# Optimization experiments

Hardware: AMD Instinct MI355X
Metric: run time of the kernel (lower is better)

Reference implementation:

```python
import jax, jax.numpy as jnp
import numpy as np
import math

B, T, C = 4, 2048, 1024
D_ATTN, N_HEAD = 1024, 16
HEAD = D_ATTN // N_HEAD


def setup_inputs() -> dict:
    key = jax.random.key(0)
    k1, k2, k3 = jax.random.split(key, 3)
    x = jax.random.normal(k1, (B, T, C), dtype=jnp.float32)
    mask = jnp.tril(jnp.ones((T, T), dtype=jnp.int32))  # causal mask, 0 = blocked
    W_qkv = jax.random.normal(k2, (C, 3 * D_ATTN), dtype=jnp.float32) * (1.0 / math.sqrt(C))
    b_qkv = jnp.zeros((3 * D_ATTN,), dtype=jnp.float32)
    W_out = jax.random.normal(k3, (D_ATTN, C), dtype=jnp.float32) * (1.0 / math.sqrt(D_ATTN))
    b_out = jnp.zeros((C,), dtype=jnp.float32)
    return {"x": x, "mask": mask, "W_qkv": W_qkv, "b_qkv": b_qkv, "W_out": W_out, "b_out": b_out}


def reference(x, mask, W_qkv, b_qkv, W_out, b_out):
    Bx, Tx, Cx = x.shape
    qkv = x @ W_qkv + b_qkv                      # [B, T, 3*d_attn]
    q, k, v = jnp.split(qkv, 3, axis=-1)
    # [B, T, d_attn] -> [B, H, T, head]
    q = q.reshape(Bx, Tx, N_HEAD, HEAD).transpose(0, 2, 1, 3)
    k = k.reshape(Bx, Tx, N_HEAD, HEAD).transpose(0, 2, 1, 3)
    v = v.reshape(Bx, Tx, N_HEAD, HEAD).transpose(0, 2, 1, 3)
    scale = 1.0 / math.sqrt(HEAD)
    scores = jnp.einsum('bhqd,bhkd->bhqk', q, k) * scale  # [B, H, T, T]
    scores = jnp.where(mask == 0, -jnp.inf, scores)
    att = jax.nn.softmax(scores, axis=-1)
    out = jnp.einsum('bhqk,bhkd->bhqd', att, v)           # [B, H, T, head]
    out = out.transpose(0, 2, 1, 3).reshape(Bx, Tx, D_ATTN)
    return out @ W_out + b_out
```

## Files before the change

kernel.cpp:

```cpp
#include <hip/hip_runtime.h>

#define B_    4
#define T_    2048
#define C_    1024
#define DATTN 1024
#define NHEAD 16
#define M_    (B_*T_)
#define NQKV  (3*DATTN)

typedef __bf16 bf16;
typedef bf16  bf16x8 __attribute__((ext_vector_type(8)));
typedef bf16  bf16x4 __attribute__((ext_vector_type(4)));
typedef short s16x4  __attribute__((ext_vector_type(4)));
typedef float f32x4  __attribute__((ext_vector_type(4)));
typedef unsigned short u16x8 __attribute__((ext_vector_type(8)));

#define NEGBIG (-1e30f)
#define QSCALE (0.125f * 1.44269504088896f)

typedef const __attribute__((address_space(1))) unsigned int* gas_u32;
typedef __attribute__((address_space(3))) unsigned int* las_u32;

static __device__ __forceinline__ f32x4 mfma16(bf16x4 a, bf16x4 b, f32x4 c) {
#if __has_builtin(__builtin_amdgcn_mfma_f32_16x16x16bf16_1k)
    return __builtin_amdgcn_mfma_f32_16x16x16bf16_1k(
        __builtin_bit_cast(s16x4, a), __builtin_bit_cast(s16x4, b), c, 0, 0, 0);
#else
    asm("v_mfma_f32_16x16x16_bf16 %0, %1, %2, %0" : "+v"(c) : "v"(a), "v"(b));
    return c;
#endif
}

static __device__ __forceinline__ bf16x4 pk4(float a, float b, float c, float d) {
    union { unsigned int u[2]; bf16x4 v; } r;
    asm("v_cvt_pk_bf16_f32 %0, %1, %2" : "=v"(r.u[0]) : "v"(a), "v"(b));
    asm("v_cvt_pk_bf16_f32 %0, %1, %2" : "=v"(r.u[1]) : "v"(c), "v"(d));
    return r.v;
}

__global__ void detect_dtype(const unsigned short* __restrict__ x, int* flag) {
    __shared__ int cnt;
    if (threadIdx.x == 0) cnt = 0;
    __syncthreads();
    int local = 0;
    for (int j = 0; j < 8; ++j) {
        u16x8 v = *(const u16x8*)&x[(j * 256 + threadIdx.x) * 8];
        for (int k = 0; k < 8; ++k)
            if ((v[k] & 0x7F80) == 0x7F80) ++local;
    }
    atomicAdd(&cnt, local);
    __syncthreads();
    if (threadIdx.x == 0) *flag = (cnt > 0) ? 1 : 0;
}

__global__ void convert_x_any(const void* __restrict__ src, bf16* __restrict__ dst,
                              int n, const int* __restrict__ flag) {
    int i = (blockIdx.x * 256 + threadIdx.x) * 8;
    if (i >= n) return;
    if (*flag == 0) {
        *(bf16x8*)&dst[i] = *(const bf16x8*)((const bf16*)src + i);
    } else {
        const float* s = (const float*)src + i;
        f32x4 a = *(const f32x4*)s, b2 = *(const f32x4*)(s + 4);
        bf16x8 r;
        r[0] = (bf16)a[0]; r[1] = (bf16)a[1]; r[2] = (bf16)a[2]; r[3] = (bf16)a[3];
        r[4] = (bf16)b2[0]; r[5] = (bf16)b2[1]; r[6] = (bf16)b2[2]; r[7] = (bf16)b2[3];
        *(bf16x8*)&dst[i] = r;
    }
}

__global__ void prep_bias(const void* __restrict__ bq, const void* __restrict__ bo,
                          bf16* __restrict__ dq, bf16* __restrict__ do_,
                          const int* __restrict__ flag) {
    const int f = *flag;
    int i = blockIdx.x * 256 + threadIdx.x;
    if (i < NQKV) {
        float v = f ? ((const float*)bq)[i] : (float)((const bf16*)bq)[i];
        if (i < DATTN) v *= QSCALE;
        dq[i] = (bf16)v;
    } else if (i - NQKV < C_) {
        do_[i - NQKV] = f ? (bf16)((const float*)bo)[i - NQKV] : ((const bf16*)bo)[i - NQKV];
    }
}

__global__ void transpose_w_any(const void* __restrict__ src, bf16* __restrict__ dst,
                                int R, int C, const int* __restrict__ flag,
                                float scale, int scale_cols) {
    __shared__ bf16 tile[32][33];
    const int f = *flag;
    const int c0 = blockIdx.x * 32, r0 = blockIdx.y * 32;
    const int tx = threadIdx.x & 31, ty = threadIdx.x >> 5;
    const float s = (c0 + tx < scale_cols) ? scale : 1.0f;
    for (int p = 0; p < 4; ++p) {
        int row = p * 8 + ty;
        size_t idx = (size_t)(r0 + row) * C + c0 + tx;
        float v = f ? ((const float*)src)[idx] : (float)((const bf16*)src)[idx];
        tile[row][tx] = (bf16)(v * s);
    }
    __syncthreads();
    for (int p = 0; p < 4; ++p) {
        int row = p * 8 + ty;
        dst[(size_t)(c0 + row) * R + r0 + tx] = tile[tx][row];
    }
}

__global__ void transpose_v(const bf16* __restrict__ qkv, bf16* __restrict__ vt) {
    __shared__ bf16 tile[32][33];
    const int t0 = blockIdx.x * 32, d0 = blockIdx.y * 32, bh = blockIdx.z;
    const int b = bh >> 4, h = bh & 15;
    const int tx = threadIdx.x & 31, ty = threadIdx.x >> 5;
    for (int p = 0; p < 4; ++p) {
        int tt = p * 8 + ty;
        tile[tt][tx] = qkv[((size_t)b * T_ + t0 + tt) * NQKV + 2 * DATTN + h * 64 + d0 + tx];
    }
    __syncthreads();
    for (int p = 0; p < 4; ++p) {
        int dd = p * 8 + ty;
        vt[((size_t)bh * 64 + d0 + dd) * T_ + t0 + tx] = tile[tx][dd];
    }
}

template<typename TC>
__global__ __launch_bounds__(256) void gemm_bt(const bf16* __restrict__ A,
                                               const bf16* __restrict__ Bt,
                                               const bf16* __restrict__ bias,
                                               TC* __restrict__ Cc,
                                               int M, int N, int K,
                                               const int* __restrict__ flag, int want) {
    if (flag && *flag != want) return;
    __shared__ __align__(16) bf16 As[128 * 64];
    __shared__ __align__(16) bf16 Bs[128 * 64];
    const int tid  = threadIdx.x;
    const int lane = tid & 63, wave = tid >> 6;
    const int quad = lane >> 4, l15 = lane & 15;
    const int wr = wave >> 1, wc = wave & 1;
    const int m0 = blockIdx.y * 128, n0 = blockIdx.x * 128;
    const int srow = lane >> 3;
    const int scol = ((lane & 7) ^ srow) * 8;
    const int l7x8 = (l15 & 7);

    f32x4 acc[4][4];
    for (int i = 0; i < 4; ++i)
        for (int j = 0; j < 4; ++j)
            acc[i][j] = f32x4{0.f, 0.f, 0.f, 0.f};

    for (int k0 = 0; k0 < K; k0 += 64) {
        for (int c = 0; c < 4; ++c) {
            int chunk = wave * 4 + c;
            int row = chunk * 8 + srow;
            __builtin_amdgcn_global_load_lds(
                (gas_u32)&A[(size_t)(m0 + row) * K + k0 + scol],
                (las_u32)&As[chunk * 512], 16, 0, 0);
            __builtin_amdgcn_global_load_lds(
                (gas_u32)&Bt[(size_t)(n0 + row) * K + k0 + scol],
                (las_u32)&Bs[chunk * 512], 16, 0, 0);
        }
        __syncthreads();
        for (int ks = 0; ks < 2; ++ks) {
            bf16x8 af[4], bfr[4];
            for (int i = 0; i < 4; ++i)
                af[i] = *(const bf16x8*)&As[(wr * 64 + i * 16 + l15) * 64 +
                                            (((ks * 4 + quad) ^ l7x8) * 8)];
            for (int j = 0; j < 4; ++j)
                bfr[j] = *(const bf16x8*)&Bs[(wc * 64 + j * 16 + l15) * 64 +
                                             (((ks * 4 + quad) ^ l7x8) * 8)];
            for (int i = 0; i < 4; ++i)
                for (int j = 0; j < 4; ++j)
                    acc[i][j] = __builtin_amdgcn_mfma_f32_16x16x32_bf16(af[i], bfr[j], acc[i][j], 0, 0, 0);
        }
        __syncthreads();
    }

    for (int i = 0; i < 4; ++i) {
        int row = m0 + wr * 64 + i * 16 + quad * 4;
        for (int j = 0; j < 4; ++j) {
            int col = n0 + wc * 64 + j * 16 + l15;
            float bv = (float)bias[col];
            for (int r = 0; r < 4; ++r) {
                float v = acc[i][j][r] + bv;
                if constexpr (__is_same(TC, float)) Cc[(size_t)(row + r) * N + col] = v;
                else                                Cc[(size_t)(row + r) * N + col] = (bf16)v;
            }
        }
    }
}

__global__ __launch_bounds__(256, 4) void attn_fused8(const bf16* __restrict__ qkv,
                                                      const bf16* __restrict__ vt,
                                                      bf16* __restrict__ out) {
    __shared__ __align__(16) bf16 Ks[2][64 * 64];
    __shared__ __align__(16) bf16 Vs[2][64 * 64];
    const int tid  = threadIdx.x;
    const int lane = tid & 63, wave = tid >> 6;
    const int quad = lane >> 4, l15 = lane & 15;
    const int srow = lane >> 3;
    const int scol = ((lane & 7) ^ srow) * 8;
    const int l7   = l15 & 7;
    const int g0   = quad >> 1, h4 = (quad & 1) * 4;
    const int bh = blockIdx.x & 63;
    const int i  = blockIdx.x >> 6;
    const int b  = bh >> 4, h = bh & 15;
    const int lo = i, hi = 31 - i;
    const size_t rowbase = (size_t)b * T_;

    const size_t koff = (size_t)(wave * 16 + srow) * NQKV + scol;
    const size_t voff = (size_t)(wave * 16 + srow) * T_ + scol;
    const bf16* kp = qkv + rowbase * NQKV + DATTN + h * 64;
    const bf16* vp = vt + (size_t)bh * 64 * T_;

    auto stage = [&](const bf16* kq, const bf16* vq, int buf) {
        for (int p = 0; p < 2; ++p) {
            int chunk = wave * 2 + p;
            __builtin_amdgcn_global_load_lds(
                (gas_u32)(kq + koff + (size_t)p * 8 * NQKV),
                (las_u32)&Ks[buf][chunk * 512], 16, 0, 0);
            __builtin_amdgcn_global_load_lds(
                (gas_u32)(vq + voff + (size_t)p * 8 * T_),
                (las_u32)&Vs[buf][chunk * 512], 16, 0, 0);
        }
    };

    bf16x8 qf[2][2];
#pragma unroll
    for (int t = 0; t < 2; ++t) {
        int q0 = (t ? hi : lo) * 64;
        size_t r = rowbase + q0 + wave * 16 + l15;
        const bf16* p = &qkv[r * NQKV + h * 64];
        qf[t][0] = *(const bf16x8*)&p[quad * 8];
        qf[t][1] = *(const bf16x8*)&p[32 + quad * 8];
    }

    bf16x4 onesf;
#pragma unroll
    for (int j = 0; j < 4; ++j) onesf[j] = (bf16)1.0f;

    f32x4 oa[2][4];
    f32x4 lac[2];
#pragma unroll
    for (int t = 0; t < 2; ++t) {
        lac[t] = f32x4{0.f, 0.f, 0.f, 0.f};
        for (int c = 0; c < 4; ++c)
            oa[t][c] = f32x4{0.f, 0.f, 0.f, 0.f};
    }

    stage(kp, vp, 0);
    kp += (size_t)64 * NQKV;
    vp += 64;

    for (int kt = 0; kt <= hi; ++kt) {
        const int k0 = kt * 64;
        const bool act0 = (kt <= lo);
        const int buf = kt & 1;
        __syncthreads();
        if (kt < hi) {
            stage(kp, vp, buf ^ 1);
            kp += (size_t)64 * NQKV;
            vp += 64;
        }

        const bf16* Kb = Ks[buf];
        const bf16* Vb = Vs[buf];

        f32x4 s0[4], s1[4];
#pragma unroll
        for (int c = 0; c < 4; ++c) {
            s0[c] = f32x4{0.f, 0.f, 0.f, 0.f};
            s1[c] = f32x4{0.f, 0.f, 0.f, 0.f};
        }
#pragma unroll
        for (int ks = 0; ks < 2; ++ks)
#pragma unroll
            for (int c = 0; c < 4; ++c) {
                bf16x8 kf = *(const bf16x8*)&Kb[(c * 16 + l15) * 64 +
                                                (((ks * 4 + quad) ^ l7) * 8)];
                if (act0) s0[c] = __builtin_amdgcn_mfma_f32_16x16x32_bf16(kf, qf[0][ks], s0[c], 0, 0, 0);
                s1[c] = __builtin_amdgcn_mfma_f32_16x16x32_bf16(kf, qf[1][ks], s1[c], 0, 0, 0);
            }

        bf16x4 paf[2][4];
#pragma unroll
        for (int t = 0; t < 2; ++t) {
            if (t == 0 && !act0) continue;
            const int q0 = (t ? hi : lo) * 64;
            const bool diag = (kt == (t ? hi : lo));
            const int qa = q0 + wave * 16 + l15;
#pragma unroll
            for (int c = 0; c < 4; ++c) {
                const int keyb = k0 + c * 16 + quad * 4;
                float pr[4];
#pragma unroll
                for (int r = 0; r < 4; ++r) {
                    float v = t ? s1[c][r] : s0[c][r];
                    if (diag && keyb + r > qa) v = NEGBIG;
                    pr[r] = __builtin_amdgcn_exp2f(v);
                }
                paf[t][c] = pk4(pr[0], pr[1], pr[2], pr[3]);
            }
        }

#pragma unroll
        for (int c = 0; c < 4; ++c) {
            if (act0) lac[0] = mfma16(paf[0][c], onesf, lac[0]);
            lac[1] = mfma16(paf[1][c], onesf, lac[1]);
        }

#pragma unroll
        for (int c = 0; c < 4; ++c)
#pragma unroll
            for (int c2 = 0; c2 < 4; ++c2) {
                bf16x4 vf = *(const bf16x4*)&Vb[(c2 * 16 + l15) * 64 +
                                                (((2 * c + g0) ^ l7) * 8) + h4];
                if (act0) oa[0][c2] = mfma16(paf[0][c], vf, oa[0][c2]);
                oa[1][c2] = mfma16(paf[1][c], vf, oa[1][c2]);
            }
    }

#pragma unroll
    for (int t = 0; t < 2; ++t) {
        int q0 = (t ? hi : lo) * 64;
        float inv[4];
#pragma unroll
        for (int r = 0; r < 4; ++r) inv[r] = 1.f / lac[t][r];
        size_t r0 = rowbase + q0 + wave * 16 + quad * 4;
#pragma unroll
        for (int c2 = 0; c2 < 4; ++c2) {
            int col = h * 64 + c2 * 16 + l15;
#pragma unroll
            for (int r = 0; r < 4; ++r)
                out[(r0 + r) * (size_t)DATTN + col] = (bf16)(oa[t][c2][r] * inv[r]);
        }
    }
}

extern "C" void kernel_launch(void* const* d_in, const int* in_sizes, int n_in,
                              void* d_out, int out_size, void* d_ws, size_t ws_size,
                              hipStream_t stream) {
    const void* x     = d_in[0];
    const void* W_qkv = d_in[2];
    const void* b_qkv = d_in[3];
    const void* W_out = d_in[4];
    const void* b_out = d_in[5];

    char* ws = (char*)d_ws;
    int*  flag    = (int*)ws;
    bf16* qkv_buf = (bf16*)(ws + 256);
    bf16* Wqkv_t  = (bf16*)(ws + 256 + 50331648);
    bf16* Wout_t  = (bf16*)(ws + 256 + 56623104);
    bf16* att_buf = (bf16*)(ws + 256 + 58720256);
    bf16* vt_buf  = (bf16*)(ws + 256 + 75497472);
    bf16* x_bf    = (bf16*)(ws + 256 + 92274688);
    bf16* bq_bf   = (bf16*)(ws + 256 + 109051904);
    bf16* bo_bf   = (bf16*)(ws + 256 + 109058048);

    detect_dtype<<<1, 256, 0, stream>>>((const unsigned short*)x, flag);

    convert_x_any<<<M_ * C_ / (256 * 8), 256, 0, stream>>>(x, x_bf, M_ * C_, flag);
    prep_bias<<<(NQKV + C_) / 256, 256, 0, stream>>>(b_qkv, b_out, bq_bf, bo_bf, flag);
    transpose_w_any<<<dim3(NQKV / 32, C_ / 32), 256, 0, stream>>>(
        W_qkv, Wqkv_t, C_, NQKV, flag, QSCALE, DATTN);
    transpose_w_any<<<dim3(C_ / 32, DATTN / 32), 256, 0, stream>>>(
        W_out, Wout_t, DATTN, C_, flag, 1.0f, 0);

    gemm_bt<bf16><<<dim3(NQKV / 128, M_ / 128), 256, 0, stream>>>(
        x_bf, Wqkv_t, bq_bf, qkv_buf, M_, NQKV, C_, nullptr, 0);

    transpose_v<<<dim3(T_ / 32, 2, B_ * NHEAD), 256, 0, stream>>>(qkv_buf, vt_buf);

    attn_fused8<<<dim3(B_ * NHEAD * 16), 256, 0, stream>>>(qkv_buf, vt_buf, att_buf);

    gemm_bt<bf16 ><<<dim3(C_ / 128, M_ / 128), 256, 0, stream>>>(
        att_buf, Wout_t, bo_bf, (bf16*)d_out, M_, C_, DATTN, flag, 0);
    gemm_bt<float><<<dim3(C_ / 128, M_ / 128), 256, 0, stream>>>(
        att_buf, Wout_t, bo_bf, (float*)d_out, M_, C_, DATTN, flag, 1);
}
```

Baseline: 282.9 us.

## Replace QKV projection GEMM with 256x256-tile, 8-wave pipelined kernel

Adds a new GEMM kernel with 256x256 output tiles, 512 threads and double-buffered LDS filled by direct global-to-LDS loads. Loads for the next k-tile are interleaved with the MFMA work on the current tile in four quarter phases separated by barriers, and the workgroup index is remapped in an XCD-aware way. The aim is more data reuse per loaded byte and better overlap of memory with compute in the QKV projection. In exchange it uses 128KB of LDS with one block per CU and many accumulator registers, so occupancy is low.

```diff
diff --git a/kernel.cpp b/kernel.cpp
--- a/kernel.cpp
+++ b/kernel.cpp
@@ -185,6 +185,179 @@
     }
 }
 
+__global__ __launch_bounds__(512, 1) void gemm256(const bf16* __restrict__ A,
+                                                  const bf16* __restrict__ Bt,
+                                                  const bf16* __restrict__ bias,
+                                                  bf16* __restrict__ Cc,
+                                                  int M, int N, int K) {
+    __shared__ __align__(16) bf16 As[2][256 * 64];
+    __shared__ __align__(16) bf16 Bs[2][256 * 64];
+    const int tid  = threadIdx.x;
+    const int lane = tid & 63, wv = tid >> 6;
+    const int quad = lane >> 4, l15 = lane & 15;
+    const int l7   = l15 & 7;
+    const int wm = wv >> 2, wn = wv & 3;
+    const int srow = lane >> 3;
+    const int scol = ((lane & 7) ^ srow) * 8;
+
+    const int cpx = gridDim.x >> 3;
+    const int wg  = (blockIdx.x & 7) * cpx + (blockIdx.x >> 3);
+    const int nbx = N >> 8;
+    const int by = wg / nbx, bx = wg % nbx;
+    const int m0 = by * 256, n0 = bx * 256;
+
+    auto stageHalf = [&](const bf16* src, int baseRow, int k0, bf16* dst) {
+#pragma unroll
+        for (int p = 0; p < 2; ++p) {
+            int chunk = wv + p * 8;
+            __builtin_amdgcn_global_load_lds(
+                (gas_u32)&src[(size_t)(baseRow + chunk * 8 + srow) * K + k0 + scol],
+                (las_u32)&dst[chunk * 512], 16, 0, 0);
+        }
+    };
+
+    f32x4 acc[8][4];
+#pragma unroll
+    for (int i = 0; i < 8; ++i)
+#pragma unroll
+        for (int j = 0; j < 4; ++j)
+            acc[i][j] = f32x4{0.f, 0.f, 0.f, 0.f};
+
+    stageHalf(A,  m0,        0, &As[0][0]);
+    stageHalf(A,  m0 + 128,  0, &As[0][8192]);
+    stageHalf(Bt, n0,        0, &Bs[0][0]);
+    stageHalf(Bt, n0 + 128,  0, &Bs[0][8192]);
+
+    const int KT = K >> 6;
+    bf16x8 af[4], bfr[4][2];
+
+    for (int kt = 0; kt < KT - 1; ++kt) {
+        const int b = kt & 1, nb = b ^ 1;
+        const int k0n = (kt + 1) * 64;
+        const bf16* Ab = As[b];
+        const bf16* Bb = Bs[b];
+
+        stageHalf(A, m0, k0n, &As[nb][0]);
+        asm volatile("s_waitcnt vmcnt(2)" ::: "memory");
+        __builtin_amdgcn_sched_barrier(0);
+        asm volatile("s_barrier" ::: "memory");
+#pragma unroll
+        for (int ks = 0; ks < 2; ++ks) {
+#pragma unroll
+            for (int i = 0; i < 4; ++i)
+                af[i] = *(const bf16x8*)&Ab[(wm * 128 + i * 16 + l15) * 64 +
+                                            (((ks * 4 + quad) ^ l7) * 8)];
+#pragma unroll
+            for (int j = 0; j < 2; ++j)
+                bfr[j][ks] = *(const bf16x8*)&Bb[(wn * 64 + j * 16 + l15) * 64 +
+                                                 (((ks * 4 + quad) ^ l7) * 8)];
+            __builtin_amdgcn_s_setprio(1);
+#pragma unroll
+            for (int i = 0; i < 4; ++i)
+#pragma unroll
+                for (int j = 0; j < 2; ++j)
+                    acc[i][j] = __builtin_amdgcn_mfma_f32_16x16x32_bf16(af[i], bfr[j][ks], acc[i][j], 0, 0, 0);
+            __builtin_amdgcn_s_setprio(0);
+        }
+        asm volatile("s_barrier" ::: "memory");
+
+        stageHalf(A, m0 + 128, k0n, &As[nb][8192]);
+#pragma unroll
+        for (int ks = 0; ks < 2; ++ks) {
+#pragma unroll
+            for (int i = 0; i < 4; ++i)
+                af[i] = *(const bf16x8*)&Ab[(wm * 128 + i * 16 + l15) * 64 +
+                                            (((ks * 4 + quad) ^ l7) * 8)];
+#pragma unroll
+            for (int j = 0; j < 2; ++j)
+                bfr[2 + j][ks] = *(const bf16x8*)&Bb[(wn * 64 + (2 + j) * 16 + l15) * 64 +
+                                                     (((ks * 4 + quad) ^ l7) * 8)];
+            __builtin_amdgcn_s_setprio(1);
+#pragma unroll
+            for (int i = 0; i < 4; ++i)
+#pragma unroll
+                for (int j = 0; j < 2; ++j)
+                    acc[i][2 + j] = __builtin_amdgcn_mfma_f32_16x16x32_bf16(af[i], bfr[2 + j][ks], acc[i][2 + j], 0, 0, 0);
+            __builtin_amdgcn_s_setprio(0);
+        }
+        asm volatile("s_barrier" ::: "memory");
+
+        stageHalf(Bt, n0, k0n, &Bs[nb][0]);
+#pragma unroll
+        for (int ks = 0; ks < 2; ++ks) {
+#pragma unroll
+            for (int i = 0; i < 4; ++i)
+                af[i] = *(const bf16x8*)&Ab[(wm * 128 + 64 + i * 16 + l15) * 64 +
+                                            (((ks * 4 + quad) ^ l7) * 8)];
+            __builtin_amdgcn_s_setprio(1);
+#pragma unroll
+            for (int i = 0; i < 4; ++i)
+#pragma unroll
+                for (int j = 0; j < 2; ++j)
+                    acc[4 + i][j] = __builtin_amdgcn_mfma_f32_16x16x32_bf16(af[i], bfr[j][ks], acc[4 + i][j], 0, 0, 0);
+            __builtin_amdgcn_s_setprio(0);
+        }
+        asm volatile("s_barrier" ::: "memory");
+
+        stageHalf(Bt, n0 + 128, k0n, &Bs[nb][8192]);
+#pragma unroll
+        for (int ks = 0; ks < 2; ++ks) {
+#pragma unroll
+            for (int i = 0; i < 4; ++i)
+                af[i] = *(const bf16x8*)&Ab[(wm * 128 + 64 + i * 16 + l15) * 64 +
+                                            (((ks * 4 + quad) ^ l7) * 8)];
+            __builtin_amdgcn_s_setprio(1);
+#pragma unroll
+            for (int i = 0; i < 4; ++i)
+#pragma unroll
+                for (int j = 0; j < 2; ++j)
+                    acc[4 + i][2 + j] = __builtin_amdgcn_mfma_f32_16x16x32_bf16(af[i], bfr[2 + j][ks], acc[4 + i][2 + j], 0, 0, 0);
+            __builtin_amdgcn_s_setprio(0);
+        }
+        asm volatile("s_barrier" ::: "memory");
+    }
+
+    {
+        const int b = (KT - 1) & 1;
+        const bf16* Ab = As[b];
+        const bf16* Bb = Bs[b];
+        asm volatile("s_waitcnt vmcnt(0)" ::: "memory");
+        __builtin_amdgcn_sched_barrier(0);
+        asm volatile("s_barrier" ::: "memory");
+#pragma unroll
+        for (int mh = 0; mh < 2; ++mh)
+#pragma unroll
+            for (int ks = 0; ks < 2; ++ks) {
+#pragma unroll
+                for (int i = 0; i < 4; ++i)
+                    af[i] = *(const bf16x8*)&Ab[(wm * 128 + mh * 64 + i * 16 + l15) * 64 +
+                                                (((ks * 4 + quad) ^ l7) * 8)];
+#pragma unroll
+                for (int j = 0; j < 4; ++j)
+                    bfr[j][ks] = *(const bf16x8*)&Bb[(wn * 64 + j * 16 + l15) * 64 +
+                                                     (((ks * 4 + quad) ^ l7) * 8)];
+#pragma unroll
+                for (int i = 0; i < 4; ++i)
+#pragma unroll
+                    for (int j = 0; j < 4; ++j)
+                        acc[mh * 4 + i][j] = __builtin_amdgcn_mfma_f32_16x16x32_bf16(af[i], bfr[j][ks], acc[mh * 4 + i][j], 0, 0, 0);
+            }
+    }
+
+#pragma unroll
+    for (int i = 0; i < 8; ++i) {
+        int row = m0 + wm * 128 + i * 16 + quad * 4;
+#pragma unroll
+        for (int j = 0; j < 4; ++j) {
+            int col = n0 + wn * 64 + j * 16 + l15;
+            float bv = (float)bias[col];
+#pragma unroll
+            for (int r = 0; r < 4; ++r)
+                Cc[(size_t)(row + r) * N + col] = (bf16)(acc[i][j][r] + bv);
+        }
+    }
+}
+
 __global__ __launch_bounds__(256, 4) void attn_fused8(const bf16* __restrict__ qkv,
                                                       const bf16* __restrict__ vt,
                                                       bf16* __restrict__ out) {
@@ -361,8 +534,8 @@
     transpose_w_any<<<dim3(C_ / 32, DATTN / 32), 256, 0, stream>>>(
         W_out, Wout_t, DATTN, C_, flag, 1.0f, 0);
 
-    gemm_bt<bf16><<<dim3(NQKV / 128, M_ / 128), 256, 0, stream>>>(
-        x_bf, Wqkv_t, bq_bf, qkv_buf, M_, NQKV, C_, nullptr, 0);
+    gemm256<<<dim3((M_ / 256) * (NQKV / 256)), 512, 0, stream>>>(
+        x_bf, Wqkv_t, bq_bf, qkv_buf, M_, NQKV, C_);
 
     transpose_v<<<dim3(T_ / 32, 2, B_ * NHEAD), 256, 0, stream>>>(qkv_buf, vt_buf);
 
```

New measurement: 314.7 us. +11.2%, slower.

## Add 256x256-tile 512-thread GEMM for QKV projection with swizzled block mapping

Applied to the files above, without the earlier changes.

Replaces the 128x128 QKV projection GEMM with a new kernel using 256x256 output tiles, 8 waves of 512 threads, double-buffered LDS staging via global_load_lds, and 16x16x32 bf16 MFMAs. Blocks are remapped so that consecutive launch slots spread across 8 groups, aimed at L2 locality. Larger tiles raise arithmetic intensity and cut global traffic, but use 128 KB of LDS per block and 128 accumulator registers per lane, which limits occupancy. The grid is only 384 blocks, so the tail over the CUs may be uneven.

```diff
diff --git a/kernel.cpp b/kernel.cpp
--- a/kernel.cpp
+++ b/kernel.cpp
@@ -185,6 +185,101 @@
     }
 }
 
+__global__ __launch_bounds__(512, 2) void gemm256b(const bf16* __restrict__ A,
+                                                   const bf16* __restrict__ Bt,
+                                                   const bf16* __restrict__ bias,
+                                                   bf16* __restrict__ Cc,
+                                                   int M, int N, int K) {
+    __shared__ __align__(16) bf16 As[2][256 * 64];
+    __shared__ __align__(16) bf16 Bs[2][256 * 64];
+    const int tid  = threadIdx.x;
+    const int lane = tid & 63, wv = tid >> 6;
+    const int quad = lane >> 4, l15 = lane & 15;
+    const int l7   = l15 & 7;
+    const int wm = wv >> 2, wn = wv & 3;
+    const int srow = lane >> 3;
+    const int scol = ((lane & 7) ^ srow) * 8;
+
+    const int cpx = gridDim.x >> 3;
+    const int wg  = (blockIdx.x & 7) * cpx + (blockIdx.x >> 3);
+    const int nbx = N >> 8;
+    const int by = wg / nbx, bx = wg % nbx;
+    const int m0 = by * 256, n0 = bx * 256;
+
+    auto stageTile = [&](const bf16* src, int baseRow, int k0, bf16* dst) {
+#pragma unroll
+        for (int p = 0; p < 4; ++p) {
+            int chunk = wv * 4 + p;
+            __builtin_amdgcn_global_load_lds(
+                (gas_u32)&src[(size_t)(baseRow + chunk * 8 + srow) * K + k0 + scol],
+                (las_u32)&dst[chunk * 512], 16, 0, 0);
+        }
+    };
+
+    f32x4 acc[8][4];
+#pragma unroll
+    for (int i = 0; i < 8; ++i)
+#pragma unroll
+        for (int j = 0; j < 4; ++j)
+            acc[i][j] = f32x4{0.f, 0.f, 0.f, 0.f};
+
+    stageTile(A,  m0, 0, &As[0][0]);
+    stageTile(Bt, n0, 0, &Bs[0][0]);
+
+    const int KT = K >> 6;
+
+    for (int kt = 0; kt < KT; ++kt) {
+        const int b = kt & 1;
+        __syncthreads();
+        if (kt + 1 < KT) {
+            stageTile(A,  m0, (kt + 1) * 64, &As[b ^ 1][0]);
+            stageTile(Bt, n0, (kt + 1) * 64, &Bs[b ^ 1][0]);
+        }
+
+        const bf16* Ab = As[b];
+        const bf16* Bb = Bs[b];
+
+        bf16x8 bfr[4][2];
+#pragma unroll
+        for (int ks = 0; ks < 2; ++ks)
+#pragma unroll
+            for (int j = 0; j < 4; ++j)
+                bfr[j][ks] = *(const bf16x8*)&Bb[(wn * 64 + j * 16 + l15) * 64 +
+                                                 (((ks * 4 + quad) ^ l7) * 8)];
+#pragma unroll
+        for (int mh = 0; mh < 2; ++mh) {
+            bf16x8 af[4][2];
+#pragma unroll
+            for (int ks = 0; ks < 2; ++ks)
+#pragma unroll
+                for (int i = 0; i < 4; ++i)
+                    af[i][ks] = *(const bf16x8*)&Ab[(wm * 128 + mh * 64 + i * 16 + l15) * 64 +
+                                                    (((ks * 4 + quad) ^ l7) * 8)];
+#pragma unroll
+            for (int ks = 0; ks < 2; ++ks)
+#pragma unroll
+                for (int i = 0; i < 4; ++i)
+#pragma unroll
+                    for (int j = 0; j < 4; ++j)
+                        acc[mh * 4 + i][j] = __builtin_amdgcn_mfma_f32_16x16x32_bf16(
+                            af[i][ks], bfr[j][ks], acc[mh * 4 + i][j], 0, 0, 0);
+        }
+    }
+
+#pragma unroll
+    for (int i = 0; i < 8; ++i) {
+        int row = m0 + wm * 128 + i * 16 + quad * 4;
+#pragma unroll
+        for (int j = 0; j < 4; ++j) {
+            int col = n0 + wn * 64 + j * 16 + l15;
+            float bv = (float)bias[col];
+#pragma unroll
+            for (int r = 0; r < 4; ++r)
+                Cc[(size_t)(row + r) * N + col] = (bf16)(acc[i][j][r] + bv);
+        }
+    }
+}
+
 __global__ __launch_bounds__(256, 4) void attn_fused8(const bf16* __restrict__ qkv,
                                                       const bf16* __restrict__ vt,
                                                       bf16* __restrict__ out) {
@@ -361,8 +456,8 @@
     transpose_w_any<<<dim3(C_ / 32, DATTN / 32), 256, 0, stream>>>(
         W_out, Wout_t, DATTN, C_, flag, 1.0f, 0);
 
-    gemm_bt<bf16><<<dim3(NQKV / 128, M_ / 128), 256, 0, stream>>>(
-        x_bf, Wqkv_t, bq_bf, qkv_buf, M_, NQKV, C_, nullptr, 0);
+    gemm256b<<<dim3((M_ / 256) * (NQKV / 256)), 512, 0, stream>>>(
+        x_bf, Wqkv_t, bq_bf, qkv_buf, M_, NQKV, C_);
 
     transpose_v<<<dim3(T_ / 32, 2, B_ * NHEAD), 256, 0, stream>>>(qkv_buf, vt_buf);
 
```

After: 292.8 us. 1.03x slower.

## Merge prep kernels into one launch and write V transposed from QKV GEMM epilogue

Applied to the files above, without the earlier changes.

Merges the x conversion, bias prep and both weight transposes into a single prep_all kernel that dispatches on block index. The separate transpose_v kernel is removed: the QKV GEMM epilogue now writes V tiles directly into the transposed vt layout, using 4-element vector stores along t. This cuts launch overhead and a full read and write pass over V. V is no longer stored in qkv_buf, which is fine only if attention reads V solely from vt. The transposed stores are strided across rows and may coalesce less well.

```diff
diff --git a/kernel.cpp b/kernel.cpp
--- a/kernel.cpp
+++ b/kernel.cpp
@@ -53,43 +53,57 @@
     if (threadIdx.x == 0) *flag = (cnt > 0) ? 1 : 0;
 }
 
-__global__ void convert_x_any(const void* __restrict__ src, bf16* __restrict__ dst,
-                              int n, const int* __restrict__ flag) {
-    int i = (blockIdx.x * 256 + threadIdx.x) * 8;
-    if (i >= n) return;
-    if (*flag == 0) {
-        *(bf16x8*)&dst[i] = *(const bf16x8*)((const bf16*)src + i);
+__global__ void prep_all(const void* __restrict__ x, bf16* __restrict__ x_bf,
+                         const void* __restrict__ bq, const void* __restrict__ bo,
+                         bf16* __restrict__ dq, bf16* __restrict__ do_,
+                         const void* __restrict__ Wq, bf16* __restrict__ Wqt,
+                         const void* __restrict__ Wo, bf16* __restrict__ Wot,
+                         const int* __restrict__ flag) {
+    __shared__ bf16 tile[32][33];
+    const int bid = blockIdx.x;
+    const int tid = threadIdx.x;
+    const int f = *flag;
+
+    if (bid < 4096) {
+        int i = (bid * 256 + tid) * 8;
+        if (f == 0) {
+            *(bf16x8*)&x_bf[i] = *(const bf16x8*)((const bf16*)x + i);
+        } else {
+            const float* s = (const float*)x + i;
+            f32x4 a = *(const f32x4*)s, b2 = *(const f32x4*)(s + 4);
+            bf16x8 r;
+            r[0] = (bf16)a[0]; r[1] = (bf16)a[1]; r[2] = (bf16)a[2]; r[3] = (bf16)a[3];
+            r[4] = (bf16)b2[0]; r[5] = (bf16)b2[1]; r[6] = (bf16)b2[2]; r[7] = (bf16)b2[3];
+            *(bf16x8*)&x_bf[i] = r;
+        }
+        return;
+    }
+    if (bid < 4112) {
+        int i = (bid - 4096) * 256 + tid;
+        if (i < NQKV) {
+            float v = f ? ((const float*)bq)[i] : (float)((const bf16*)bq)[i];
+            if (i < DATTN) v *= QSCALE;
+            dq[i] = (bf16)v;
+        } else if (i - NQKV < C_) {
+            do_[i - NQKV] = f ? (bf16)((const float*)bo)[i - NQKV]
+                              : ((const bf16*)bo)[i - NQKV];
+        }
+        return;
+    }
+
+    const void* src; bf16* dst; int R, C, c0, r0; float scale; int scale_cols;
+    if (bid < 7184) {
+        int id = bid - 4112;
+        src = Wq; dst = Wqt; R = C_; C = NQKV;
+        c0 = (id % (NQKV / 32)) * 32; r0 = (id / (NQKV / 32)) * 32;
+        scale = QSCALE; scale_cols = DATTN;
     } else {
-        const float* s = (const float*)src + i;
-        f32x4 a = *(const f32x4*)s, b2 = *(const f32x4*)(s + 4);
-        bf16x8 r;
-        r[0] = (bf16)a[0]; r[1] = (bf16)a[1]; r[2] = (bf16)a[2]; r[3] = (bf16)a[3];
-        r[4] = (bf16)b2[0]; r[5] = (bf16)b2[1]; r[6] = (bf16)b2[2]; r[7] = (bf16)b2[3];
-        *(bf16x8*)&dst[i] = r;
-    }
-}
-
-__global__ void prep_bias(const void* __restrict__ bq, const void* __restrict__ bo,
-                          bf16* __restrict__ dq, bf16* __restrict__ do_,
-                          const int* __restrict__ flag) {
-    const int f = *flag;
-    int i = blockIdx.x * 256 + threadIdx.x;
-    if (i < NQKV) {
-        float v = f ? ((const float*)bq)[i] : (float)((const bf16*)bq)[i];
-        if (i < DATTN) v *= QSCALE;
-        dq[i] = (bf16)v;
-    } else if (i - NQKV < C_) {
-        do_[i - NQKV] = f ? (bf16)((const float*)bo)[i - NQKV] : ((const bf16*)bo)[i - NQKV];
-    }
-}
-
-__global__ void transpose_w_any(const void* __restrict__ src, bf16* __restrict__ dst,
-                                int R, int C, const int* __restrict__ flag,
-                                float scale, int scale_cols) {
-    __shared__ bf16 tile[32][33];
-    const int f = *flag;
-    const int c0 = blockIdx.x * 32, r0 = blockIdx.y * 32;
-    const int tx = threadIdx.x & 31, ty = threadIdx.x >> 5;
+        int id = bid - 7184;
+        src = Wo; dst = Wot; R = DATTN; C = C_;
+        c0 = (id % (C_ / 32)) * 32; r0 = (id / (C_ / 32)) * 32;
+        scale = 1.0f; scale_cols = 0;
+    }
+    const int tx = tid & 31, ty = tid >> 5;
     const float s = (c0 + tx < scale_cols) ? scale : 1.0f;
     for (int p = 0; p < 4; ++p) {
         int row = p * 8 + ty;
@@ -104,29 +118,14 @@
     }
 }
 
-__global__ void transpose_v(const bf16* __restrict__ qkv, bf16* __restrict__ vt) {
-    __shared__ bf16 tile[32][33];
-    const int t0 = blockIdx.x * 32, d0 = blockIdx.y * 32, bh = blockIdx.z;
-    const int b = bh >> 4, h = bh & 15;
-    const int tx = threadIdx.x & 31, ty = threadIdx.x >> 5;
-    for (int p = 0; p < 4; ++p) {
-        int tt = p * 8 + ty;
-        tile[tt][tx] = qkv[((size_t)b * T_ + t0 + tt) * NQKV + 2 * DATTN + h * 64 + d0 + tx];
-    }
-    __syncthreads();
-    for (int p = 0; p < 4; ++p) {
-        int dd = p * 8 + ty;
-        vt[((size_t)bh * 64 + d0 + dd) * T_ + t0 + tx] = tile[tx][dd];
-    }
-}
-
 template<typename TC>
 __global__ __launch_bounds__(256) void gemm_bt(const bf16* __restrict__ A,
                                                const bf16* __restrict__ Bt,
                                                const bf16* __restrict__ bias,
                                                TC* __restrict__ Cc,
                                                int M, int N, int K,
-                                               const int* __restrict__ flag, int want) {
+                                               const int* __restrict__ flag, int want,
+                                               bf16* __restrict__ vt) {
     if (flag && *flag != want) return;
     __shared__ __align__(16) bf16 As[128 * 64];
     __shared__ __align__(16) bf16 Bs[128 * 64];
@@ -169,6 +168,23 @@
                     acc[i][j] = __builtin_amdgcn_mfma_f32_16x16x32_bf16(af[i], bfr[j], acc[i][j], 0, 0, 0);
         }
         __syncthreads();
+    }
+
+    if (vt && n0 >= 2 * DATTN) {
+        for (int i = 0; i < 4; ++i) {
+            int row = m0 + wr * 64 + i * 16 + quad * 4;
+            int batch = row >> 11, t = row & (T_ - 1);
+            for (int j = 0; j < 4; ++j) {
+                int cg = n0 + wc * 64 + j * 16 + l15;
+                int vcol = cg - 2 * DATTN;
+                int h = vcol >> 6, d = vcol & 63;
+                float bv = (float)bias[cg];
+                bf16x4 o;
+                for (int r = 0; r < 4; ++r) o[r] = (bf16)(acc[i][j][r] + bv);
+                *(bf16x4*)&vt[((size_t)(batch * 16 + h) * 64 + d) * T_ + t] = o;
+            }
+        }
+        return;
     }
 
     for (int i = 0; i < 4; ++i) {
@@ -354,22 +370,16 @@
 
     detect_dtype<<<1, 256, 0, stream>>>((const unsigned short*)x, flag);
 
-    convert_x_any<<<M_ * C_ / (256 * 8), 256, 0, stream>>>(x, x_bf, M_ * C_, flag);
-    prep_bias<<<(NQKV + C_) / 256, 256, 0, stream>>>(b_qkv, b_out, bq_bf, bo_bf, flag);
-    transpose_w_any<<<dim3(NQKV / 32, C_ / 32), 256, 0, stream>>>(
-        W_qkv, Wqkv_t, C_, NQKV, flag, QSCALE, DATTN);
-    transpose_w_any<<<dim3(C_ / 32, DATTN / 32), 256, 0, stream>>>(
-        W_out, Wout_t, DATTN, C_, flag, 1.0f, 0);
+    prep_all<<<8208, 256, 0, stream>>>(x, x_bf, b_qkv, b_out, bq_bf, bo_bf,
+                                       W_qkv, Wqkv_t, W_out, Wout_t, flag);
 
     gemm_bt<bf16><<<dim3(NQKV / 128, M_ / 128), 256, 0, stream>>>(
-        x_bf, Wqkv_t, bq_bf, qkv_buf, M_, NQKV, C_, nullptr, 0);
-
-    transpose_v<<<dim3(T_ / 32, 2, B_ * NHEAD), 256, 0, stream>>>(qkv_buf, vt_buf);
+        x_bf, Wqkv_t, bq_bf, qkv_buf, M_, NQKV, C_, nullptr, 0, vt_buf);
 
     attn_fused8<<<dim3(B_ * NHEAD * 16), 256, 0, stream>>>(qkv_buf, vt_buf, att_buf);
 
     gemm_bt<bf16 ><<<dim3(C_ / 128, M_ / 128), 256, 0, stream>>>(
-        att_buf, Wout_t, bo_bf, (bf16*)d_out, M_, C_, DATTN, flag, 0);
+        att_buf, Wout_t, bo_bf, (bf16*)d_out, M_, C_, DATTN, flag, 0, nullptr);
     gemm_bt<float><<<dim3(C_ / 128, M_ / 128), 256, 0, stream>>>(
-        att_buf, Wout_t, bo_bf, (float*)d_out, M_, C_, DATTN, flag, 1);
-}
+        att_buf, Wout_t, bo_bf, (float*)d_out, M_, C_, DATTN, flag, 1, nullptr);
+}
```

Result: faster. 272.0 us (-3.9%).
